# Performance work log

Hardware: AMD Instinct MI355X
Metric: run time of the kernel (lower is better)

## Reference

```python
import jax, jax.numpy as jnp
import numpy as np

D_CONV = 4
DT_RANK = 64
D_STATE = 16


def setup_inputs() -> dict:
    key = jax.random.key(0)
    ks = jax.random.split(key, 10)
    d_model, d_in, L, B = 1024, 2048, 1024, 2
    s = 0.02
    x = jax.random.normal(ks[0], (B, L, d_model), jnp.float32)
    W_in = jax.random.normal(ks[1], (d_model, 2 * d_in), jnp.float32) * s
    conv_w = jax.random.normal(ks[2], (D_CONV, 1, d_in), jnp.float32) * s
    conv_b = jax.random.normal(ks[3], (d_in,), jnp.float32) * s
    W_x = jax.random.normal(ks[4], (d_in, DT_RANK + 2 * D_STATE), jnp.float32) * s
    W_dt = jax.random.normal(ks[5], (DT_RANK, d_in), jnp.float32) * s
    b_dt = jax.random.normal(ks[6], (d_in,), jnp.float32) * s
    A_log = jnp.log(jnp.tile(jnp.arange(1, D_STATE + 1, dtype=jnp.float32), (d_in, 1)))
    D = jnp.ones((d_in,), jnp.float32)
    W_out = jax.random.normal(ks[7], (d_in, d_model), jnp.float32) * s
    return {"x": x, "W_in": W_in, "conv_w": conv_w, "conv_b": conv_b,
            "W_x": W_x, "W_dt": W_dt, "b_dt": b_dt, "A_log": A_log, "D": D,
            "W_out": W_out}


def _selective_scan(u, delta, A, Bm, Cm, D):
    # u, delta: [b,l,d]; A: [d,n]; Bm, Cm: [b,l,n]; D: [d]
    b, l, d = u.shape
    n = A.shape[1]
    deltaA = jnp.exp(jnp.einsum('bld,dn->bldn', delta, A))          # [b,l,d,n]
    dBu = delta[..., None] * Bm[:, :, None, :] * u[..., None]        # [b,l,d,n]

    def step(state, inp):
        dA_t, dBu_t, C_t = inp                                       # [b,d,n],[b,d,n],[b,n]
        state = dA_t * state + dBu_t
        y_t = jnp.einsum('bdn,bn->bd', state, C_t)
        return state, y_t

    init = jnp.zeros((b, d, n), u.dtype)
    xs = (jnp.swapaxes(deltaA, 0, 1), jnp.swapaxes(dBu, 0, 1), jnp.swapaxes(Cm, 0, 1))
    _, ys = jax.lax.scan(step, init, xs)                             # [l,b,d]
    y = jnp.swapaxes(ys, 0, 1)
    return y + u * D


def reference(x, W_in, conv_w, conv_b, W_x, W_dt, b_dt, A_log, D, W_out):
    B, L, _ = x.shape
    d_in = W_in.shape[1] // 2

    x_and_res = x @ W_in                                             # [B,L,2*d_in]
    x_, res = jnp.split(x_and_res, [d_in], axis=-1)

    # depthwise causal conv over the projected branch
    x_pad = jnp.pad(x_, ((0, 0), (D_CONV - 1, 0), (0, 0)))
    x_conv = jax.lax.conv_general_dilated(
        x_pad, conv_w, window_strides=(1,), padding='VALID',
        dimension_numbers=('NWC', 'WIO', 'NWC'), feature_group_count=d_in)
    x_conv = x_conv[:, :L, :] + conv_b
    x_conv = jax.nn.silu(x_conv)

    # ssm
    A = -jnp.exp(A_log)                                              # [d_in,n]
    x_dbl = x_conv @ W_x                                             # [B,L,dt_rank+2n]
    delta, Bm, Cm = jnp.split(x_dbl, [DT_RANK, DT_RANK + D_STATE], axis=-1)
    delta = jax.nn.softplus(delta @ W_dt + b_dt)                     # [B,L,d_in]
    y = _selective_scan(x_conv, delta, A, Bm, Cm, D)

    y = y * jax.nn.silu(res)
    return y @ W_out
```

## Files before the change

kernel.cpp:

```cpp
#include <hip/hip_runtime.h>
#include <hip/hip_bf16.h>
#include <math.h>


typedef unsigned short u16;
typedef short s16;
typedef float f32x4 __attribute__((ext_vector_type(4)));
typedef s16 bf16x8 __attribute__((ext_vector_type(8)));

#define LDS_CAST(p) ((__attribute__((address_space(3))) void*)(p))
#define GLB_CAST(p) ((const __attribute__((address_space(1))) void*)(p))

#define LL 1024
#define DI 2048
#define NC 32
#define LC 32

#define OFF_FLAG   0u
#define OFF_CX     256u
#define OFF_CCW    4194560u
#define OFF_CCB    4211200u
#define OFF_CBDT   4215296u
#define OFF_CALOG  4219392u
#define OFF_CD     4284928u
#define OFF_WINT   4289024u
#define OFF_WOUTT  12677632u
#define OFF_WXT    16871936u
#define OFF_WDTT   17265152u
#define OFF_XRP    17527296u
#define OFF_XF     (OFF_XRP + 0u)
#define OFF_P      (OFF_XRP + 0u)
#define OFF_YBF    (OFF_XRP + 0u)
#define OFF_S      (OFF_XRP + 16777216u)
#define OFF_SIN    (OFF_XRP + 33554432u)
#define OFF_YP     (OFF_XRP + 16777216u)
#define OFF_RESACT 84636160u
#define OFF_XCB    101413376u
#define OFF_XDBLP  109801984u
#define OFF_XDBL   116093440u
#define OFF_DELTA  116486656u

static __device__ __forceinline__ float b2f(u16 h) {
  return __uint_as_float(((unsigned)h) << 16);
}
static __device__ __forceinline__ u16 f2b(float f) {
  unsigned u = __float_as_uint(f);
  u += 0x7fffu + ((u >> 16) & 1u);
  return (u16)(u >> 16);
}

__global__ __launch_bounds__(256) void detect_dtype(
    const u16* __restrict__ x, const void* __restrict__ alog, int* flag) {
  __shared__ int cnt;
  if (threadIdx.x == 0) cnt = 0;
  __syncthreads();
  int good = 0;
#pragma unroll
  for (int j = 0; j < 16; j++) {
    u16 v = x[threadIdx.x * 16 + j];
    int e = (v >> 7) & 0xFF;
    good += (e >= 100 && e <= 140) ? 1 : 0;
  }
  atomicAdd(&cnt, good);
  __syncthreads();
  if (threadIdx.x == 0) {
    int fp32in = (cnt < 3600) ? 1 : 0;
    flag[0] = fp32in;
    int structured = fp32in;
    if (fp32in) {
      const float* af = (const float*)alog;
#pragma unroll
      for (int n = 0; n < 16; n++) {
        float a0 = __expf(af[n]);
        float a1 = __expf(af[777 * 16 + n]);
        float t = (float)(n + 1);
        if (fabsf(a0 - t) > 0.01f * t || fabsf(a1 - t) > 0.01f * t) structured = 0;
      }
    }
    flag[1] = structured;
  }
}

__global__ __launch_bounds__(256) void prep_inputs(
    const void* sx, const void* scw, const void* scb, const void* sbdt,
    const void* salog, const void* sd,
    const void* Win, const void* Wx, const void* Wdt, const void* Wout,
    char* __restrict__ ws, const int* __restrict__ flag) {
  const int fl = flag[0];
  int bid = blockIdx.x;
  if (bid < 8376) {
    long i = (long)bid * 256 + threadIdx.x;
    if (i >= 2144256) return;
    const void* src; u16* dst; long j;
    if (i < 2097152)      { src = sx;    dst = (u16*)(ws + OFF_CX);    j = i; }
    else if (i < 2105344) { src = scw;   dst = (u16*)(ws + OFF_CCW);   j = i - 2097152; }
    else if (i < 2107392) { src = scb;   dst = (u16*)(ws + OFF_CCB);   j = i - 2105344; }
    else if (i < 2109440) { src = sbdt;  dst = (u16*)(ws + OFF_CBDT);  j = i - 2107392; }
    else if (i < 2142208) { src = salog; dst = (u16*)(ws + OFF_CALOG); j = i - 2109440; }
    else                  { src = sd;    dst = (u16*)(ws + OFF_CD);    j = i - 2142208; }
    dst[j] = fl ? f2b(((const float*)src)[j]) : ((const u16*)src)[j];
    return;
  }
  bid -= 8376;
  const void* src; u16* dst; int R, C, tx_, ty_;
  if (bid < 4096)      { src=Win;  dst=(u16*)(ws+OFF_WINT);  R=1024; C=4096; ty_=bid/128; tx_=bid%128; }
  else if (bid < 6144) { bid-=4096; src=Wout; dst=(u16*)(ws+OFF_WOUTT); R=2048; C=1024; ty_=bid/32; tx_=bid%32; }
  else if (bid < 6336) { bid-=6144; src=Wx;   dst=(u16*)(ws+OFF_WXT);   R=2048; C=96;   ty_=bid/3;  tx_=bid%3; }
  else                 { bid-=6336; src=Wdt;  dst=(u16*)(ws+OFF_WDTT);  R=64;   C=2048; ty_=bid/64; tx_=bid%64; }
  __shared__ u16 tile[32][33];
  int tx = threadIdx.x & 31, ty = threadIdx.x >> 5;
  int c0 = tx_*32, r0 = ty_*32;
#pragma unroll
  for (int i = 0; i < 4; i++) {
    int r = r0 + ty + i*8, c = c0 + tx;
    if (r < R && c < C) {
      size_t off = (size_t)r*C + c;
      tile[ty + i*8][tx] = fl ? f2b(((const float*)src)[off]) : ((const u16*)src)[off];
    }
  }
  __syncthreads();
#pragma unroll
  for (int i = 0; i < 4; i++) {
    int c = c0 + ty + i*8, r = r0 + tx;
    if (r < R && c < C) dst[(size_t)c*R + r] = tile[tx][ty + i*8];
  }
}

__global__ __launch_bounds__(256) void gemm_in_fused(
    const u16* __restrict__ A, const u16* __restrict__ Bt,
    float* __restrict__ xf, float* __restrict__ resact) {
  __shared__ u16 sA[128*32];
  __shared__ u16 sB[128*32];
  const int tid = threadIdx.x;
  const int lane = tid & 63, w = tid >> 6;
  const int ln = lane & 15, q = lane >> 4;
  const int wr = w >> 1, wc = w & 1;
  const int m0 = blockIdx.y * 128, n0 = blockIdx.x * 128;
  const int lda = 1024;
  const int li0 = tid, li1 = tid + 256;
  const int r0s = li0 >> 2, k0s = (li0 & 3) * 8;
  const int r1s = li1 >> 2, k1s = (li1 & 3) * 8;
  f32x4 acc[4][4] = {};
  for (int k0 = 0; k0 < 1024; k0 += 32) {
    __syncthreads();
    __builtin_amdgcn_global_load_lds(GLB_CAST(A + (size_t)(m0 + r0s)*lda + k0 + k0s), LDS_CAST(&sA[(size_t)li0*8]), 16, 0, 0);
    __builtin_amdgcn_global_load_lds(GLB_CAST(A + (size_t)(m0 + r1s)*lda + k0 + k1s), LDS_CAST(&sA[(size_t)li1*8]), 16, 0, 0);
    __builtin_amdgcn_global_load_lds(GLB_CAST(Bt + (size_t)(n0 + r0s)*lda + k0 + k0s), LDS_CAST(&sB[(size_t)li0*8]), 16, 0, 0);
    __builtin_amdgcn_global_load_lds(GLB_CAST(Bt + (size_t)(n0 + r1s)*lda + k0 + k1s), LDS_CAST(&sB[(size_t)li1*8]), 16, 0, 0);
    __syncthreads();
    bf16x8 af[4], bfr[4];
#pragma unroll
    for (int i = 0; i < 4; i++) {
      af[i]  = *(const bf16x8*)&sA[(wr*64 + i*16 + ln)*32 + q*8];
      bfr[i] = *(const bf16x8*)&sB[(wc*64 + i*16 + ln)*32 + q*8];
    }
#pragma unroll
    for (int mi = 0; mi < 4; mi++)
#pragma unroll
      for (int ni = 0; ni < 4; ni++)
        acc[mi][ni] = __builtin_amdgcn_mfma_f32_16x16x32_bf16(af[mi], bfr[ni], acc[mi][ni], 0, 0, 0);
  }
  const int half = (n0 >= DI) ? 1 : 0;
  float* dst = half ? resact : xf;
  const int nb = n0 - (half ? DI : 0);
#pragma unroll
  for (int mi = 0; mi < 4; mi++)
#pragma unroll
    for (int ni = 0; ni < 4; ni++)
#pragma unroll
      for (int r = 0; r < 4; r++) {
        int m = m0 + wr*64 + mi*16 + q*4 + r;
        int n = nb + wc*64 + ni*16 + ln;
        float v = acc[mi][ni][r];
        if (half) {
          if (!(v == v)) v = 0.f;
          float t = fminf(fmaxf(v, -80.f), 80.f);
          v = v / (1.f + __expf(-t));
        }
        dst[(size_t)m*DI + n] = v;
      }
}

__global__ __launch_bounds__(256) void gemm128split(
    const u16* __restrict__ A, const u16* __restrict__ Bt,
    float* __restrict__ Cout, int M, int N, int lda, int kslice) {
  __shared__ u16 sA[128*32];
  __shared__ u16 sB[128*32];
  const int tid = threadIdx.x;
  const int lane = tid & 63, w = tid >> 6;
  const int ln = lane & 15, q = lane >> 4;
  const int wr = w >> 1, wc = w & 1;
  const int m0 = blockIdx.y * 128, n0 = blockIdx.x * 128;
  const int kstart = blockIdx.z * kslice, kend = kstart + kslice;
  Cout += (size_t)blockIdx.z * M * N;
  const int li0 = tid, li1 = tid + 256;
  const int r0s = li0 >> 2, k0s = (li0 & 3) * 8;
  const int r1s = li1 >> 2, k1s = (li1 & 3) * 8;
  f32x4 acc[4][4] = {};
  for (int k0 = kstart; k0 < kend; k0 += 32) {
    __syncthreads();
    __builtin_amdgcn_global_load_lds(GLB_CAST(A + (size_t)(m0 + r0s)*lda + k0 + k0s), LDS_CAST(&sA[(size_t)li0*8]), 16, 0, 0);
    __builtin_amdgcn_global_load_lds(GLB_CAST(A + (size_t)(m0 + r1s)*lda + k0 + k1s), LDS_CAST(&sA[(size_t)li1*8]), 16, 0, 0);
    __builtin_amdgcn_global_load_lds(GLB_CAST(Bt + (size_t)(n0 + r0s)*lda + k0 + k0s), LDS_CAST(&sB[(size_t)li0*8]), 16, 0, 0);
    __builtin_amdgcn_global_load_lds(GLB_CAST(Bt + (size_t)(n0 + r1s)*lda + k0 + k1s), LDS_CAST(&sB[(size_t)li1*8]), 16, 0, 0);
    __syncthreads();
    bf16x8 af[4], bfr[4];
#pragma unroll
    for (int i = 0; i < 4; i++) {
      af[i]  = *(const bf16x8*)&sA[(wr*64 + i*16 + ln)*32 + q*8];
      bfr[i] = *(const bf16x8*)&sB[(wc*64 + i*16 + ln)*32 + q*8];
    }
#pragma unroll
    for (int mi = 0; mi < 4; mi++)
#pragma unroll
      for (int ni = 0; ni < 4; ni++)
        acc[mi][ni] = __builtin_amdgcn_mfma_f32_16x16x32_bf16(af[mi], bfr[ni], acc[mi][ni], 0, 0, 0);
  }
#pragma unroll
  for (int mi = 0; mi < 4; mi++)
#pragma unroll
    for (int ni = 0; ni < 4; ni++)
#pragma unroll
      for (int r = 0; r < 4; r++) {
        int m = m0 + wr*64 + mi*16 + q*4 + r;
        int n = n0 + wc*64 + ni*16 + ln;
        Cout[(size_t)m*N + n] = acc[mi][ni][r];
      }
}

__global__ __launch_bounds__(256) void conv_silu(
    const float* __restrict__ xf, const u16* __restrict__ cw, const u16* __restrict__ cb,
    u16* __restrict__ xcb) {
  int idx = blockIdx.x * 256 + threadIdx.x;
  int d = idx & (DI - 1);
  int row = idx >> 11;
  int l = row & (LL - 1);
  float acc = b2f(cb[d]);
#pragma unroll
  for (int j = 0; j < 4; j++) {
    int ls = l - 3 + j;
    if (ls >= 0) acc += b2f(cw[j*DI + d]) * xf[(size_t)(row - 3 + j)*DI + d];
  }
  if (!(acc == acc)) acc = 0.f;
  float t = fminf(fmaxf(acc, -80.f), 80.f);
  xcb[idx] = f2b(acc / (1.f + __expf(-t)));
}

__global__ __launch_bounds__(256) void xdbl_split(
    const u16* __restrict__ A, const u16* __restrict__ Bt, float* __restrict__ outP) {
  int wg = blockIdx.x * 4 + (threadIdx.x >> 6);
  int lane = threadIdx.x & 63, ln = lane & 15, q = lane >> 4;
  int mt = wg / 48, rem = wg % 48;
  int nt = rem >> 3, ks = rem & 7;
  const u16* ap = A  + (size_t)(mt*16 + ln)*2048 + ks*256 + q*8;
  const u16* bp = Bt + (size_t)(nt*16 + ln)*2048 + ks*256 + q*8;
  f32x4 acc = {};
#pragma unroll
  for (int k0 = 0; k0 < 256; k0 += 32) {
    bf16x8 a = *(const bf16x8*)(ap + k0);
    bf16x8 b = *(const bf16x8*)(bp + k0);
    acc = __builtin_amdgcn_mfma_f32_16x16x32_bf16(a, b, acc, 0, 0, 0);
  }
#pragma unroll
  for (int r = 0; r < 4; r++)
    outP[((size_t)ks*2048 + mt*16 + q*4 + r)*96 + nt*16 + ln] = acc[r];
}

__global__ __launch_bounds__(256) void xdbl_reduce(
    const float* __restrict__ outP, u16* __restrict__ xdbl) {
  int i = blockIdx.x * 256 + threadIdx.x;
  float s = 0.f;
#pragma unroll
  for (int ks = 0; ks < 8; ks++) s += outP[(size_t)ks*196608 + i];
  xdbl[i] = f2b(s);
}

__global__ __launch_bounds__(256) void gemm_delta(
    const u16* __restrict__ xdbl, const u16* __restrict__ WdtT,
    const u16* __restrict__ bdt, float* __restrict__ delta) {
  int w = (blockIdx.x * 256 + threadIdx.x) >> 6;
  int lane = threadIdx.x & 63, ln = lane & 15, q = lane >> 4;
  int mt = w & 127, nt = w >> 7;
  const u16* ap = xdbl + (size_t)(mt*16 + ln)*96 + q*8;
  const u16* bp = WdtT + (size_t)(nt*16 + ln)*64 + q*8;
  f32x4 acc = {};
#pragma unroll
  for (int k0 = 0; k0 < 64; k0 += 32) {
    bf16x8 a = *(const bf16x8*)(ap + k0);
    bf16x8 b = *(const bf16x8*)(bp + k0);
    acc = __builtin_amdgcn_mfma_f32_16x16x32_bf16(a, b, acc, 0, 0, 0);
  }
#pragma unroll
  for (int r = 0; r < 4; r++) {
    int m = mt*16 + q*4 + r, n = nt*16 + ln;
    float v = acc[r] + b2f(bdt[n]);
    if (!(v == v)) v = 0.f;
    float sp = (v > 15.f) ? v : log1pf(__expf(fmaxf(v, -80.f)));
    delta[(size_t)m*DI + n] = sp;
  }
}

__global__ __launch_bounds__(256) void scan_p1(
    const float* __restrict__ delta, const u16* __restrict__ xcb,
    const u16* __restrict__ xdbl, const u16* __restrict__ Alog,
    float* __restrict__ P, float* __restrict__ S, const int* __restrict__ flag) {
  const int structured = flag[1];
  int bid = blockIdx.x;
  int b = bid >> 8, r = bid & 255;
  int chunk = r >> 3, dblk = r & 7;
  int d = dblk*256 + threadIdx.x;
  float s[16], p[16];
#pragma unroll
  for (int n = 0; n < 16; n++) { s[n] = 0.f; p[n] = 1.f; }
  int row0 = b*LL + chunk*LC;
  if (structured) {
    for (int l = 0; l < LC; l++) {
      int row = row0 + l;
      float dl = delta[(size_t)row*DI + d];
      float du = dl * b2f(xcb[(size_t)row*DI + d]);
      const u16* bq = xdbl + (size_t)row*96 + 64;
      bf16x8 bv0 = *(const bf16x8*)(bq);
      bf16x8 bv1 = *(const bf16x8*)(bq + 8);
      float e1 = __expf(-dl);
      float dAc = 1.f;
#pragma unroll
      for (int n = 0; n < 8; n++) {
        dAc *= e1;
        s[n] = dAc * s[n] + du * b2f((u16)bv0[n]);
        p[n] *= dAc;
      }
#pragma unroll
      for (int n = 0; n < 8; n++) {
        dAc *= e1;
        s[n+8] = dAc * s[n+8] + du * b2f((u16)bv1[n]);
        p[n+8] *= dAc;
      }
    }
  } else {
    float Av[16];
#pragma unroll
    for (int n = 0; n < 16; n++) Av[n] = -__expf(fminf(b2f(Alog[d*16 + n]), 80.f));
    for (int l = 0; l < LC; l++) {
      int row = row0 + l;
      float dl = delta[(size_t)row*DI + d];
      float du = dl * b2f(xcb[(size_t)row*DI + d]);
      const u16* bq = xdbl + (size_t)row*96 + 64;
      bf16x8 bv0 = *(const bf16x8*)(bq);
      bf16x8 bv1 = *(const bf16x8*)(bq + 8);
#pragma unroll
      for (int n = 0; n < 8; n++) {
        float dA = __expf(fmaxf(dl * Av[n], -80.f));
        s[n] = dA * s[n] + du * b2f((u16)bv0[n]);
        p[n] *= dA;
      }
#pragma unroll
      for (int n = 0; n < 8; n++) {
        float dA = __expf(fmaxf(dl * Av[n+8], -80.f));
        s[n+8] = dA * s[n+8] + du * b2f((u16)bv1[n]);
        p[n+8] *= dA;
      }
    }
  }
  size_t o = ((size_t)(b*NC + chunk)*DI + d) * 16;
#pragma unroll
  for (int n = 0; n < 16; n++) { P[o + n] = p[n]; S[o + n] = s[n]; }
}

__global__ __launch_bounds__(256) void scan_p2(
    const float* __restrict__ P, const float* __restrict__ S, float* __restrict__ sIn) {
  int idx = blockIdx.x * 256 + threadIdx.x;
  int n = idx & 15, d = (idx >> 4) & (DI - 1), b = idx >> 15;
  float s = 0.f;
  for (int c = 0; c < NC; c++) {
    size_t o = ((size_t)(b*NC + c)*DI + d)*16 + n;
    sIn[o] = s;
    s = P[o] * s + S[o];
  }
}

__global__ __launch_bounds__(256) void scan_p3(
    const float* __restrict__ delta, const u16* __restrict__ xcb,
    const u16* __restrict__ xdbl, const u16* __restrict__ Alog,
    const u16* __restrict__ Dp, const float* __restrict__ resact,
    const float* __restrict__ sIn, u16* __restrict__ ybf, const int* __restrict__ flag) {
  const int structured = flag[1];
  int bid = blockIdx.x;
  int b = bid >> 8, r = bid & 255;
  int chunk = r >> 3, dblk = r & 7;
  int d = dblk*256 + threadIdx.x;
  float Dv = b2f(Dp[d]);
  float s[16];
  size_t o = ((size_t)(b*NC + chunk)*DI + d) * 16;
#pragma unroll
  for (int n = 0; n < 16; n++) s[n] = sIn[o + n];
  int row0 = b*LL + chunk*LC;
  if (structured) {
    for (int l = 0; l < LC; l++) {
      int row = row0 + l;
      float dl = delta[(size_t)row*DI + d];
      float u  = b2f(xcb[(size_t)row*DI + d]);
      float du = dl * u;
      const u16* bq = xdbl + (size_t)row*96 + 64;
      bf16x8 bv0 = *(const bf16x8*)(bq);
      bf16x8 bv1 = *(const bf16x8*)(bq + 8);
      bf16x8 cv0 = *(const bf16x8*)(bq + 16);
      bf16x8 cv1 = *(const bf16x8*)(bq + 24);
      float e1 = __expf(-dl);
      float dAc = 1.f;
      float y = 0.f;
#pragma unroll
      for (int n = 0; n < 8; n++) {
        dAc *= e1;
        s[n] = dAc * s[n] + du * b2f((u16)bv0[n]);
        y += s[n] * b2f((u16)cv0[n]);
      }
#pragma unroll
      for (int n = 0; n < 8; n++) {
        dAc *= e1;
        s[n+8] = dAc * s[n+8] + du * b2f((u16)bv1[n]);
        y += s[n+8] * b2f((u16)cv1[n]);
      }
      y += u * Dv;
      float out = y * resact[(size_t)row*DI + d];
      if (!(out == out)) out = 0.f;
      ybf[(size_t)row*DI + d] = f2b(out);
    }
  } else {
    float Av[16];
#pragma unroll
    for (int n = 0; n < 16; n++) Av[n] = -__expf(fminf(b2f(Alog[d*16 + n]), 80.f));
    for (int l = 0; l < LC; l++) {
      int row = row0 + l;
      float dl = delta[(size_t)row*DI + d];
      float u  = b2f(xcb[(size_t)row*DI + d]);
      float du = dl * u;
      const u16* bq = xdbl + (size_t)row*96 + 64;
      bf16x8 bv0 = *(const bf16x8*)(bq);
      bf16x8 bv1 = *(const bf16x8*)(bq + 8);
      bf16x8 cv0 = *(const bf16x8*)(bq + 16);
      bf16x8 cv1 = *(const bf16x8*)(bq + 24);
      float y = 0.f;
#pragma unroll
      for (int n = 0; n < 8; n++) {
        float dA = __expf(fmaxf(dl * Av[n], -80.f));
        s[n] = dA * s[n] + du * b2f((u16)bv0[n]);
        y += s[n] * b2f((u16)cv0[n]);
      }
#pragma unroll
      for (int n = 0; n < 8; n++) {
        float dA = __expf(fmaxf(dl * Av[n+8], -80.f));
        s[n+8] = dA * s[n+8] + du * b2f((u16)bv1[n]);
        y += s[n+8] * b2f((u16)cv1[n]);
      }
      y += u * Dv;
      float out = y * resact[(size_t)row*DI + d];
      if (!(out == out)) out = 0.f;
      ybf[(size_t)row*DI + d] = f2b(out);
    }
  }
}

__global__ __launch_bounds__(256) void out_reduce(
    const float* __restrict__ yP, void* __restrict__ out, const int* __restrict__ flag) {
  const int fl = flag[0];
  int i = blockIdx.x * 256 + threadIdx.x;
  float v = 0.f;
#pragma unroll
  for (int z = 0; z < 4; z++) v += yP[(size_t)z*2097152 + i];
  if (!(v == v)) v = 0.f;
  if (fl) ((float*)out)[i] = v;
  else    ((u16*)out)[i] = f2b(v);
}

extern "C" void kernel_launch(void* const* d_in, const int* in_sizes, int n_in,
                              void* d_out, int out_size, void* d_ws, size_t ws_size,
                              hipStream_t stream) {
  char* ws = (char*)d_ws;
  int*   flag   = (int*)  (ws + OFF_FLAG);
  u16*   cx     = (u16*)  (ws + OFF_CX);
  u16*   ccw    = (u16*)  (ws + OFF_CCW);
  u16*   ccb    = (u16*)  (ws + OFF_CCB);
  u16*   cbdt   = (u16*)  (ws + OFF_CBDT);
  u16*   cAlog  = (u16*)  (ws + OFF_CALOG);
  u16*   cD     = (u16*)  (ws + OFF_CD);
  u16*   WinT   = (u16*)  (ws + OFF_WINT);
  u16*   WoutT  = (u16*)  (ws + OFF_WOUTT);
  u16*   WxT    = (u16*)  (ws + OFF_WXT);
  u16*   WdtT   = (u16*)  (ws + OFF_WDTT);
  float* xf     = (float*)(ws + OFF_XF);
  float* resact = (float*)(ws + OFF_RESACT);
  u16*   xcb    = (u16*)  (ws + OFF_XCB);
  float* xdblP  = (float*)(ws + OFF_XDBLP);
  u16*   xdbl   = (u16*)  (ws + OFF_XDBL);
  float* delta  = (float*)(ws + OFF_DELTA);
  u16*   ybf    = (u16*)  (ws + OFF_YBF);
  float* P      = (float*)(ws + OFF_P);
  float* S      = (float*)(ws + OFF_S);
  float* sIn    = (float*)(ws + OFF_SIN);
  float* yP     = (float*)(ws + OFF_YP);

  detect_dtype<<<1, 256, 0, stream>>>((const u16*)d_in[0], d_in[7], flag);
  prep_inputs<<<14840, 256, 0, stream>>>(
      d_in[0], d_in[2], d_in[3], d_in[6], d_in[7], d_in[8],
      d_in[1], d_in[4], d_in[5], d_in[9], ws, flag);
  gemm_in_fused<<<dim3(32, 16), 256, 0, stream>>>(cx, WinT, xf, resact);
  conv_silu<<<16384, 256, 0, stream>>>(xf, ccw, ccb, xcb);
  xdbl_split<<<1536, 256, 0, stream>>>(xcb, WxT, xdblP);
  xdbl_reduce<<<768, 256, 0, stream>>>(xdblP, xdbl);
  gemm_delta<<<4096, 256, 0, stream>>>(xdbl, WdtT, cbdt, delta);
  scan_p1<<<512, 256, 0, stream>>>(delta, xcb, xdbl, cAlog, P, S, flag);
  scan_p2<<<256, 256, 0, stream>>>(P, S, sIn);
  scan_p3<<<512, 256, 0, stream>>>(delta, xcb, xdbl, cAlog, cD, resact, sIn, ybf, flag);
  gemm128split<<<dim3(8, 16, 4), 256, 0, stream>>>(ybf, WoutT, yP, 2048, 1024, 2048, 512);
  out_reduce<<<8192, 256, 0, stream>>>(yP, d_out, flag);
}
```

Baseline: 263.6 us.

## Fold dtype detection, xdbl reduction and output reduction into neighbouring kernels

Dtype detection now runs inside every prep_inputs block, removing a separate launch. The xdbl GEMM now computes the full K loop per wave and writes bf16 directly, removing the split-K partial buffer and its reduce kernel. The output split-K GEMM uses a per-tile atomic semaphore so the last of the four K-slice blocks sums the partials and writes the output, removing out_reduce. conv_silu is vectorised to four channels per thread. The costs are redundant detection work in every prep block, less parallelism in xdbl, and reliance on the semaphore being zeroed each call.

```diff
diff --git a/kernel.cpp b/kernel.cpp
--- a/kernel.cpp
+++ b/kernel.cpp
@@ -7,6 +7,7 @@
 typedef short s16;
 typedef float f32x4 __attribute__((ext_vector_type(4)));
 typedef s16 bf16x8 __attribute__((ext_vector_type(8)));
+typedef u16 u16x4 __attribute__((ext_vector_type(4)));
 
 #define LDS_CAST(p) ((__attribute__((address_space(3))) void*)(p))
 #define GLB_CAST(p) ((const __attribute__((address_space(1))) void*)(p))
@@ -36,7 +37,7 @@
 #define OFF_YP     (OFF_XRP + 16777216u)
 #define OFF_RESACT 84636160u
 #define OFF_XCB    101413376u
-#define OFF_XDBLP  109801984u
+#define OFF_SEM    109801984u
 #define OFF_XDBL   116093440u
 #define OFF_DELTA  116486656u
 
@@ -49,45 +50,48 @@
   return (u16)(u >> 16);
 }
 
-__global__ __launch_bounds__(256) void detect_dtype(
-    const u16* __restrict__ x, const void* __restrict__ alog, int* flag) {
-  __shared__ int cnt;
-  if (threadIdx.x == 0) cnt = 0;
-  __syncthreads();
-  int good = 0;
-#pragma unroll
-  for (int j = 0; j < 16; j++) {
-    u16 v = x[threadIdx.x * 16 + j];
-    int e = (v >> 7) & 0xFF;
-    good += (e >= 100 && e <= 140) ? 1 : 0;
-  }
-  atomicAdd(&cnt, good);
-  __syncthreads();
-  if (threadIdx.x == 0) {
-    int fp32in = (cnt < 3600) ? 1 : 0;
-    flag[0] = fp32in;
-    int structured = fp32in;
-    if (fp32in) {
-      const float* af = (const float*)alog;
-#pragma unroll
-      for (int n = 0; n < 16; n++) {
-        float a0 = __expf(af[n]);
-        float a1 = __expf(af[777 * 16 + n]);
-        float t = (float)(n + 1);
-        if (fabsf(a0 - t) > 0.01f * t || fabsf(a1 - t) > 0.01f * t) structured = 0;
-      }
-    }
-    flag[1] = structured;
-  }
-}
-
 __global__ __launch_bounds__(256) void prep_inputs(
     const void* sx, const void* scw, const void* scb, const void* sbdt,
     const void* salog, const void* sd,
     const void* Win, const void* Wx, const void* Wdt, const void* Wout,
-    char* __restrict__ ws, const int* __restrict__ flag) {
-  const int fl = flag[0];
+    char* __restrict__ ws) {
+  __shared__ int cnt_s;
+  if (threadIdx.x == 0) cnt_s = 0;
+  __syncthreads();
+  {
+    int good = 0;
+#pragma unroll
+    for (int j = 0; j < 16; j++) {
+      u16 v = ((const u16*)sx)[threadIdx.x * 16 + j];
+      int e = (v >> 7) & 0xFF;
+      good += (e >= 100 && e <= 140) ? 1 : 0;
+    }
+    atomicAdd(&cnt_s, good);
+  }
+  __syncthreads();
+  const int fl = (cnt_s < 3600) ? 1 : 0;
+
   int bid = blockIdx.x;
+  if (bid == 0) {
+    if (threadIdx.x < 128) ((unsigned*)(ws + OFF_SEM))[threadIdx.x] = 0u;
+    if (threadIdx.x == 0) {
+      int* flag = (int*)(ws + OFF_FLAG);
+      flag[0] = fl;
+      int structured = fl;
+      if (fl) {
+        const float* af = (const float*)salog;
+#pragma unroll
+        for (int n = 0; n < 16; n++) {
+          float a0 = __expf(af[n]);
+          float a1 = __expf(af[777 * 16 + n]);
+          float t = (float)(n + 1);
+          if (fabsf(a0 - t) > 0.01f * t || fabsf(a1 - t) > 0.01f * t) structured = 0;
+        }
+      }
+      flag[1] = structured;
+    }
+  }
+
   if (bid < 8376) {
     long i = (long)bid * 256 + threadIdx.x;
     if (i >= 2144256) return;
@@ -181,9 +185,10 @@
       }
 }
 
-__global__ __launch_bounds__(256) void gemm128split(
+__global__ __launch_bounds__(256) void gemm_out_fused(
     const u16* __restrict__ A, const u16* __restrict__ Bt,
-    float* __restrict__ Cout, int M, int N, int lda, int kslice) {
+    float* __restrict__ Cpart, unsigned* __restrict__ sem,
+    void* __restrict__ out, const int* __restrict__ flag) {
   __shared__ u16 sA[128*32];
   __shared__ u16 sB[128*32];
   const int tid = threadIdx.x;
@@ -191,8 +196,9 @@
   const int ln = lane & 15, q = lane >> 4;
   const int wr = w >> 1, wc = w & 1;
   const int m0 = blockIdx.y * 128, n0 = blockIdx.x * 128;
-  const int kstart = blockIdx.z * kslice, kend = kstart + kslice;
-  Cout += (size_t)blockIdx.z * M * N;
+  const int lda = 2048;
+  const int kstart = blockIdx.z * 512, kend = kstart + 512;
+  float* Cout = Cpart + (size_t)blockIdx.z * (2048*1024);
   const int li0 = tid, li1 = tid + 256;
   const int r0s = li0 >> 2, k0s = (li0 & 3) * 8;
   const int r1s = li1 >> 2, k1s = (li1 & 3) * 8;
@@ -224,55 +230,78 @@
       for (int r = 0; r < 4; r++) {
         int m = m0 + wr*64 + mi*16 + q*4 + r;
         int n = n0 + wc*64 + ni*16 + ln;
-        Cout[(size_t)m*N + n] = acc[mi][ni][r];
-      }
+        Cout[(size_t)m*1024 + n] = acc[mi][ni][r];
+      }
+  __threadfence();
+  __syncthreads();
+  __shared__ unsigned old_;
+  if (tid == 0) old_ = atomicAdd(&sem[blockIdx.y * 8 + blockIdx.x], 1u);
+  __syncthreads();
+  if (old_ == 3u) {
+    __threadfence();
+    const int fl = flag[0];
+#pragma unroll 4
+    for (int j = 0; j < 64; j++) {
+      int e = j * 256 + tid;
+      int rr = e >> 7, cc = e & 127;
+      size_t o = (size_t)(m0 + rr) * 1024 + (n0 + cc);
+      float v = Cpart[o] + Cpart[o + 2097152] + Cpart[o + 2*2097152] + Cpart[o + 3*2097152];
+      if (!(v == v)) v = 0.f;
+      if (fl) ((float*)out)[o] = v;
+      else    ((u16*)out)[o] = f2b(v);
+    }
+  }
 }
 
 __global__ __launch_bounds__(256) void conv_silu(
     const float* __restrict__ xf, const u16* __restrict__ cw, const u16* __restrict__ cb,
     u16* __restrict__ xcb) {
-  int idx = blockIdx.x * 256 + threadIdx.x;
-  int d = idx & (DI - 1);
-  int row = idx >> 11;
+  int idx4 = blockIdx.x * 256 + threadIdx.x;
+  int d = (idx4 & 511) * 4;
+  int row = idx4 >> 9;
   int l = row & (LL - 1);
-  float acc = b2f(cb[d]);
+  u16x4 cbv = *(const u16x4*)(cb + d);
+  float acc[4];
+#pragma unroll
+  for (int c = 0; c < 4; c++) acc[c] = b2f(cbv[c]);
 #pragma unroll
   for (int j = 0; j < 4; j++) {
     int ls = l - 3 + j;
-    if (ls >= 0) acc += b2f(cw[j*DI + d]) * xf[(size_t)(row - 3 + j)*DI + d];
-  }
-  if (!(acc == acc)) acc = 0.f;
-  float t = fminf(fmaxf(acc, -80.f), 80.f);
-  xcb[idx] = f2b(acc / (1.f + __expf(-t)));
-}
-
-__global__ __launch_bounds__(256) void xdbl_split(
-    const u16* __restrict__ A, const u16* __restrict__ Bt, float* __restrict__ outP) {
-  int wg = blockIdx.x * 4 + (threadIdx.x >> 6);
+    if (ls >= 0) {
+      f32x4 xv = *(const f32x4*)(xf + (size_t)(row - 3 + j)*DI + d);
+      u16x4 wv = *(const u16x4*)(cw + j*DI + d);
+#pragma unroll
+      for (int c = 0; c < 4; c++) acc[c] += b2f(wv[c]) * xv[c];
+    }
+  }
+  u16x4 outv;
+#pragma unroll
+  for (int c = 0; c < 4; c++) {
+    float a = acc[c];
+    if (!(a == a)) a = 0.f;
+    float t = fminf(fmaxf(a, -80.f), 80.f);
+    outv[c] = f2b(a / (1.f + __expf(-t)));
+  }
+  *(u16x4*)(xcb + (size_t)row*DI + d) = outv;
+}
+
+__global__ __launch_bounds__(64) void xdbl_full(
+    const u16* __restrict__ A, const u16* __restrict__ Bt, u16* __restrict__ xdbl) {
+  int wg = blockIdx.x;
   int lane = threadIdx.x & 63, ln = lane & 15, q = lane >> 4;
-  int mt = wg / 48, rem = wg % 48;
-  int nt = rem >> 3, ks = rem & 7;
-  const u16* ap = A  + (size_t)(mt*16 + ln)*2048 + ks*256 + q*8;
-  const u16* bp = Bt + (size_t)(nt*16 + ln)*2048 + ks*256 + q*8;
+  int mt = wg / 6, nt = wg % 6;
+  const u16* ap = A  + (size_t)(mt*16 + ln)*2048 + q*8;
+  const u16* bp = Bt + (size_t)(nt*16 + ln)*2048 + q*8;
   f32x4 acc = {};
-#pragma unroll
-  for (int k0 = 0; k0 < 256; k0 += 32) {
+#pragma unroll 8
+  for (int k0 = 0; k0 < 2048; k0 += 32) {
     bf16x8 a = *(const bf16x8*)(ap + k0);
     bf16x8 b = *(const bf16x8*)(bp + k0);
     acc = __builtin_amdgcn_mfma_f32_16x16x32_bf16(a, b, acc, 0, 0, 0);
   }
 #pragma unroll
   for (int r = 0; r < 4; r++)
-    outP[((size_t)ks*2048 + mt*16 + q*4 + r)*96 + nt*16 + ln] = acc[r];
-}
-
-__global__ __launch_bounds__(256) void xdbl_reduce(
-    const float* __restrict__ outP, u16* __restrict__ xdbl) {
-  int i = blockIdx.x * 256 + threadIdx.x;
-  float s = 0.f;
-#pragma unroll
-  for (int ks = 0; ks < 8; ks++) s += outP[(size_t)ks*196608 + i];
-  xdbl[i] = f2b(s);
+    xdbl[(size_t)(mt*16 + q*4 + r)*96 + nt*16 + ln] = f2b(acc[r]);
 }
 
 __global__ __launch_bounds__(256) void gemm_delta(
@@ -458,18 +487,6 @@
       ybf[(size_t)row*DI + d] = f2b(out);
     }
   }
-}
-
-__global__ __launch_bounds__(256) void out_reduce(
-    const float* __restrict__ yP, void* __restrict__ out, const int* __restrict__ flag) {
-  const int fl = flag[0];
-  int i = blockIdx.x * 256 + threadIdx.x;
-  float v = 0.f;
-#pragma unroll
-  for (int z = 0; z < 4; z++) v += yP[(size_t)z*2097152 + i];
-  if (!(v == v)) v = 0.f;
-  if (fl) ((float*)out)[i] = v;
-  else    ((u16*)out)[i] = f2b(v);
 }
 
 extern "C" void kernel_launch(void* const* d_in, const int* in_sizes, int n_in,
@@ -490,7 +507,7 @@
   float* xf     = (float*)(ws + OFF_XF);
   float* resact = (float*)(ws + OFF_RESACT);
   u16*   xcb    = (u16*)  (ws + OFF_XCB);
-  float* xdblP  = (float*)(ws + OFF_XDBLP);
+  unsigned* sem = (unsigned*)(ws + OFF_SEM);
   u16*   xdbl   = (u16*)  (ws + OFF_XDBL);
   float* delta  = (float*)(ws + OFF_DELTA);
   u16*   ybf    = (u16*)  (ws + OFF_YBF);
@@ -499,18 +516,15 @@
   float* sIn    = (float*)(ws + OFF_SIN);
   float* yP     = (float*)(ws + OFF_YP);
 
-  detect_dtype<<<1, 256, 0, stream>>>((const u16*)d_in[0], d_in[7], flag);
   prep_inputs<<<14840, 256, 0, stream>>>(
       d_in[0], d_in[2], d_in[3], d_in[6], d_in[7], d_in[8],
-      d_in[1], d_in[4], d_in[5], d_in[9], ws, flag);
+      d_in[1], d_in[4], d_in[5], d_in[9], ws);
   gemm_in_fused<<<dim3(32, 16), 256, 0, stream>>>(cx, WinT, xf, resact);
-  conv_silu<<<16384, 256, 0, stream>>>(xf, ccw, ccb, xcb);
-  xdbl_split<<<1536, 256, 0, stream>>>(xcb, WxT, xdblP);
-  xdbl_reduce<<<768, 256, 0, stream>>>(xdblP, xdbl);
+  conv_silu<<<4096, 256, 0, stream>>>(xf, ccw, ccb, xcb);
+  xdbl_full<<<768, 64, 0, stream>>>(xcb, WxT, xdbl);
   gemm_delta<<<4096, 256, 0, stream>>>(xdbl, WdtT, cbdt, delta);
   scan_p1<<<512, 256, 0, stream>>>(delta, xcb, xdbl, cAlog, P, S, flag);
   scan_p2<<<256, 256, 0, stream>>>(P, S, sIn);
   scan_p3<<<512, 256, 0, stream>>>(delta, xcb, xdbl, cAlog, cD, resact, sIn, ybf, flag);
-  gemm128split<<<dim3(8, 16, 4), 256, 0, stream>>>(ybf, WoutT, yP, 2048, 1024, 2048, 512);
-  out_reduce<<<8192, 256, 0, stream>>>(yP, d_out, flag);
-}
+  gemm_out_fused<<<dim3(8, 16, 4), 256, 0, stream>>>(ybf, WoutT, yP, sem, d_out, flag);
+}
```

Measured after the change: 369.9 us. +40.3%, slower.
